# Performance work log

Hardware: AMD Instinct MI355X
Metric: run time of the kernel (lower is better)

The kernel has to match this reference:

```python
import jax, jax.numpy as jnp
import numpy as np

B, C, H, W = 4, 256, 64, 64

def _conv1x1(x, w, b):
    # x: [B,C,H,W], w: [O,C] (1x1 conv kernel squeezed), b: [O]
    return jnp.einsum('bchw,oc->bohw', x, w) + b[None, :, None, None]

def setup_inputs() -> dict:
    key = jax.random.key(0)
    ks = jax.random.split(key, 9)
    s = 1.0 / np.sqrt(C)
    inp = {'x': jax.random.normal(ks[0], (B, C, H, W), dtype=jnp.float32)}
    for i, name in enumerate(['f', 'g', 'h', 'v']):
        inp['W' + name] = jax.random.uniform(ks[1 + 2 * i], (C, C), jnp.float32, -s, s)
        inp['b' + name] = jax.random.uniform(ks[2 + 2 * i], (C,), jnp.float32, -s, s)
    return inp

def reference(x, Wf, bf, Wg, bg, Wh, bh, Wv, bv):
    b, c, h, w = x.shape
    n = h * w
    f = _conv1x1(x, Wf, bf).reshape(b, c, n)  # [B,C,N]
    g = _conv1x1(x, Wg, bg).reshape(b, c, n)  # [B,C,N]
    hh = _conv1x1(x, Wh, bh).reshape(b, c, n)  # [B,C,N]
    fg = jnp.einsum('bci,bcj->bij', f, g)      # [B,N,N], no scaling (as in source)
    attn = jax.nn.softmax(fg, axis=1)          # softmax over dim=1 (first N axis)
    fgh = jnp.einsum('bci,bij->bcj', hh, attn) # [B,C,N]
    return _conv1x1(fgh.reshape(b, c, h, w), Wv, bv)
```

## Files before the change

kernel.cpp:

```cpp
#include <hip/hip_runtime.h>
#include <hip/hip_bf16.h>


typedef short short8 __attribute__((ext_vector_type(8)));
typedef short short4v __attribute__((ext_vector_type(4)));
typedef float f32x4 __attribute__((ext_vector_type(4)));
typedef _Float16 f16x8 __attribute__((ext_vector_type(8)));
typedef unsigned short u16;
typedef unsigned int u32;

#define DEV static __device__ __forceinline__
#define MFMA16(a, b, c) __builtin_amdgcn_mfma_f32_16x16x32_f16(a, b, c, 0, 0, 0)

DEV u16 h16(float x) {
    union { _Float16 h; u16 u; } c;
    c.h = (_Float16)x;
    return c.u;
}
DEV f16x8 ldh8(const u16* p) { return *reinterpret_cast<const f16x8*>(p); }

DEV u32 cvtpk(float a, float b) {
    u32 r;
    asm("v_cvt_pkrtz_f16_f32 %0, %1, %2" : "=v"(r) : "v"(a), "v"(b));
    return r;
}

DEV void gload16(const void* g, void* l) {
    __builtin_amdgcn_global_load_lds(
        (const __attribute__((address_space(1))) unsigned int*)g,
        (__attribute__((address_space(3))) unsigned int*)l, 16, 0, 0);
}

constexpr size_t OFF_WF = 0;
constexpr size_t OFF_WG = 131072;
constexpr size_t OFF_WH = 262144;
constexpr size_t OFF_WV = 393216;
constexpr size_t OFF_ML = 524288;
constexpr size_t OFF_F  = 1310720;
constexpr size_t OFF_G  = OFF_F + 8388608;
constexpr size_t OFF_H  = OFF_G + 8388608;
constexpr size_t OFF_XT = OFF_H + 8388608;
constexpr size_t OFF_OP = OFF_XT;
constexpr size_t OFF_OT = OFF_F;

__global__ __launch_bounds__(256) void k_prep_w(
    const float* __restrict__ Wf, const float* __restrict__ Wg,
    const float* __restrict__ Wh, const float* __restrict__ Wv,
    u16* WF, u16* WG, u16* WH, u16* WV) {
    int i = blockIdx.x * 256 + threadIdx.x;
    WF[i] = h16(Wf[i]);
    WG[i] = h16(Wg[i]);
    WH[i] = h16(Wh[i]);
    WV[i] = h16(Wv[i]);
}

__global__ __launch_bounds__(256) void k_prep_x(const float* __restrict__ x, u16* Xt) {
    __shared__ float lds[64][65];
    int bid = blockIdx.x;
    int b = bid >> 8, rem = bid & 255, ct = rem >> 6, nt = rem & 63;
    int tid = threadIdx.x;
    int tx = tid & 63, ty = tid >> 6;
    const float* src = x + ((size_t)(b * 256 + ct * 64)) * 4096 + nt * 64;
#pragma unroll
    for (int k = 0; k < 16; ++k) {
        int cl = ty * 16 + k;
        lds[cl][tx] = src[(size_t)cl * 4096 + tx];
    }
    __syncthreads();
    int nl = tid >> 2, cg = tid & 3;
    short8 h0, h1;
#pragma unroll
    for (int j = 0; j < 8; ++j) h0[j] = (short)h16(lds[cg * 16 + j][nl]);
#pragma unroll
    for (int j = 8; j < 16; ++j) h1[j - 8] = (short)h16(lds[cg * 16 + j][nl]);
    size_t dst = ((size_t)(b * 4096 + nt * 64 + nl)) * 256 + ct * 64 + cg * 16;
    *reinterpret_cast<short8*>(Xt + dst) = h0;
    *reinterpret_cast<short8*>(Xt + dst + 8) = h1;
}

__global__ __launch_bounds__(256) void k_conv_fg(
    const u16* __restrict__ Xt, const u16* __restrict__ WF, const u16* __restrict__ WG,
    const float* __restrict__ bf, const float* __restrict__ bg,
    u16* F, u16* G) {
    int bidm = blockIdx.x & 255, bido = blockIdx.x >> 8;
    int w = threadIdx.x >> 6, lane = threadIdx.x & 63, r = lane & 15, g = lane >> 4;
    int m0 = bidm * 64 + w * 16, o0 = bido * 64;
    f32x4 fa[4], ga[4];
#pragma unroll
    for (int i = 0; i < 4; ++i) { fa[i] = {0.f, 0.f, 0.f, 0.f}; ga[i] = {0.f, 0.f, 0.f, 0.f}; }
    const u16* ar = Xt + (size_t)(m0 + r) * 256;
#pragma unroll
    for (int ks = 0; ks < 8; ++ks) {
        int k0 = ks * 32 + 8 * g;
        f16x8 a = ldh8(ar + k0);
#pragma unroll
        for (int ot = 0; ot < 4; ++ot) {
            size_t wrow = (size_t)(o0 + ot * 16 + r) * 256 + k0;
            fa[ot] = MFMA16(a, ldh8(WF + wrow), fa[ot]);
            ga[ot] = MFMA16(a, ldh8(WG + wrow), ga[ot]);
        }
    }
#pragma unroll
    for (int ot = 0; ot < 4; ++ot) {
#pragma unroll
        for (int q = 0; q < 4; ++q) {
            int row = m0 + 4 * g + q;
            int col = o0 + ot * 16 + r;
            size_t idx = (size_t)row * 256 + col;
            F[idx] = h16(fa[ot][q] + bf[col]);
            G[idx] = h16(ga[ot][q] + bg[col]);
        }
    }
}

__global__ __launch_bounds__(256) void k_conv_h(
    const u16* __restrict__ WH, const u16* __restrict__ Xt,
    const float* __restrict__ bh, u16* Hb) {
    int bidn = blockIdx.x & 255, bido = blockIdx.x >> 8;
    int w = threadIdx.x >> 6, lane = threadIdx.x & 63, r = lane & 15, g = lane >> 4;
    int o0 = bido * 64 + w * 16, n0 = bidn * 64;
    f32x4 acc[4];
#pragma unroll
    for (int i = 0; i < 4; ++i) acc[i] = {0.f, 0.f, 0.f, 0.f};
    const u16* arow = WH + (size_t)(o0 + r) * 256;
#pragma unroll
    for (int ks = 0; ks < 8; ++ks) {
        int k0 = ks * 32 + 8 * g;
        f16x8 a = ldh8(arow + k0);
#pragma unroll
        for (int ntl = 0; ntl < 4; ++ntl) {
            f16x8 bb = ldh8(Xt + (size_t)(n0 + ntl * 16 + r) * 256 + k0);
            acc[ntl] = MFMA16(a, bb, acc[ntl]);
        }
    }
#pragma unroll
    for (int ntl = 0; ntl < 4; ++ntl) {
#pragma unroll
        for (int q = 0; q < 4; ++q) {
            int o = o0 + 4 * g + q;
            int nf = n0 + ntl * 16 + r;
            int bb = nf >> 12, n = nf & 4095;
            int k5 = n & 31;
            int kp = (k5 < 16) ? (8 * (k5 >> 2) + (k5 & 3))
                               : (8 * ((k5 - 16) >> 2) + 4 + (k5 & 3));
            int np = (n & ~31) | kp;
            Hb[((size_t)(bb * 256 + o)) * 4096 + np] = h16(acc[ntl][q] + bh[o]);
        }
    }
}

__global__ __launch_bounds__(256, 2) void k_attn(
    const u16* __restrict__ F, const u16* __restrict__ G,
    const u16* __restrict__ Hb, u16* __restrict__ OP, float* __restrict__ ML) {
    __shared__ u16 Kd[2][8192];
    __shared__ u16 Vd[2][8192];

    int bid = blockIdx.x;
    int xcd = bid & 7, idx = bid >> 3;
    int b = xcd >> 1, ks = xcd & 1;
    int tid = threadIdx.x;
    int w = tid >> 6, lane = tid & 63, r = lane & 15, g = lane >> 4;
    int j0 = idx * 64 + w * 16;
    const float L2E = 1.4426950408889634f;

    int vlc = (r >> 1) * 128 + (((16 * g) + (r & 1) * 64) ^ (((r >> 1) & 7) << 4));

    f16x8 Qf[8];
    {
        const u16* q = G + (size_t)(b * 4096 + j0 + r) * 256;
#pragma unroll
        for (int k = 0; k < 8; ++k) Qf[k] = ldh8(q + k * 32 + 8 * g);
    }
    f32x4 O[16];
#pragma unroll
    for (int i = 0; i < 16; ++i) O[i] = {0.f, 0.f, 0.f, 0.f};
    float m = -1e30f, l = 0.f;

    const char* Fb  = (const char*)(F + (size_t)b * 4096 * 256);
    const char* Hbb = (const char*)(Hb + (size_t)b * 256 * 4096);

    int ksrc[4], vsrc[4];
#pragma unroll
    for (int t = 0; t < 4; ++t) {
        int d = (w * 4 + t) * 1024 + lane * 16;
        int row = d >> 9, col = d & 511;
        ksrc[t] = row * 512 + (col ^ ((row & 7) << 4));
        int r128 = d >> 7, wn = d & 127;
        int wp = wn ^ ((r128 & 7) << 4);
        vsrc[t] = ((r128 * 2 + (wp >> 6)) << 13) + (wp & 63);
    }

#define STAGE(bufn, I0)                                                         \
    do {                                                                        \
        const char* kb_ = Fb + (size_t)(I0) * 512;                              \
        const char* vb_ = Hbb + (size_t)(I0) * 2;                               \
        char* kl = (char*)Kd[bufn];                                             \
        char* vl = (char*)Vd[bufn];                                             \
        _Pragma("unroll") for (int t = 0; t < 4; ++t)                           \
            gload16(kb_ + ksrc[t], kl + (w * 4 + t) * 1024);                    \
        _Pragma("unroll") for (int t = 0; t < 4; ++t)                           \
            gload16(vb_ + vsrc[t], vl + (w * 4 + t) * 1024);                    \
    } while (0)

    int i0beg = ks * 2048;
    STAGE(0, i0beg);
    __syncthreads();

    for (int it = 0; it < 64; ++it) {
        int cur = it & 1;
        if (it + 1 < 64) STAGE(cur ^ 1, i0beg + (it + 1) * 32);

        const char* Kl = (const char*)Kd[cur];
        const char* Vb = (const char*)Vd[cur] + vlc;

        f32x4 s0 = {0.f, 0.f, 0.f, 0.f};
        f32x4 s1 = {0.f, 0.f, 0.f, 0.f};
        __builtin_amdgcn_s_setprio(1);
        {
            const char* kr = Kl + r * 512;
            int sw = (r & 7) << 4;
#pragma unroll
            for (int k = 0; k < 8; ++k) {
                f16x8 ka = *reinterpret_cast<const f16x8*>(kr + ((k * 64 + 16 * g) ^ sw));
                s0 = MFMA16(ka, Qf[k], s0);
            }
        }
        {
            const char* kr = Kl + (16 + r) * 512;
            int sw = (r & 7) << 4;
#pragma unroll
            for (int k = 0; k < 8; ++k) {
                f16x8 ka = *reinterpret_cast<const f16x8*>(kr + ((k * 64 + 16 * g) ^ sw));
                s1 = MFMA16(ka, Qf[k], s1);
            }
        }
        __builtin_amdgcn_s_setprio(0);

        float v = fmaxf(fmaxf(fmaxf(s0[0], s0[1]), fmaxf(s0[2], s0[3])),
                        fmaxf(fmaxf(s1[0], s1[1]), fmaxf(s1[2], s1[3])));
        v = fmaxf(v, __shfl_xor(v, 16));
        v = fmaxf(v, __shfl_xor(v, 32));
        float grow = v - m;
        if (__all(grow <= 8.0f)) {
#pragma unroll
            for (int q = 0; q < 4; ++q) {
                s0[q] = exp2f((s0[q] - m) * L2E);
                s1[q] = exp2f((s1[q] - m) * L2E);
            }
            l += (s0[0] + s0[1] + s0[2] + s0[3]) + (s1[0] + s1[1] + s1[2] + s1[3]);
        } else {
            float mn = fmaxf(m, v);
            float corr = exp2f((m - mn) * L2E);
            m = mn;
#pragma unroll
            for (int q = 0; q < 4; ++q) {
                s0[q] = exp2f((s0[q] - m) * L2E);
                s1[q] = exp2f((s1[q] - m) * L2E);
            }
            l = l * corr + (s0[0] + s0[1] + s0[2] + s0[3]) + (s1[0] + s1[1] + s1[2] + s1[3]);
#pragma unroll
            for (int ct = 0; ct < 16; ++ct) O[ct] *= corr;
        }

        union { u32 wd[4]; f16x8 fr; } pu;
        pu.wd[0] = cvtpk(s0[0], s0[1]);
        pu.wd[1] = cvtpk(s0[2], s0[3]);
        pu.wd[2] = cvtpk(s1[0], s1[1]);
        pu.wd[3] = cvtpk(s1[2], s1[3]);

        __builtin_amdgcn_s_setprio(1);
#pragma unroll
        for (int ct = 0; ct < 16; ++ct) {
            f16x8 vb = *reinterpret_cast<const f16x8*>(Vb + ct * 1024);
            O[ct] = MFMA16(vb, pu.fr, O[ct]);
        }
        __builtin_amdgcn_s_setprio(0);

        __syncthreads();
    }
#undef STAGE

    l += __shfl_xor(l, 16);
    l += __shfl_xor(l, 32);
    float inv = 1.f / l;
    size_t mrow = (size_t)ks * 16384 + b * 4096 + j0 + r;
#pragma unroll
    for (int ct = 0; ct < 16; ++ct) {
        short4v pk;
#pragma unroll
        for (int q = 0; q < 4; ++q) pk[q] = (short)h16(O[ct][q] * inv);
        *reinterpret_cast<short4v*>(OP + mrow * 256 + ct * 16 + 4 * g) = pk;
    }
    if (g == 0) {
        size_t mi = mrow * 2;
        ML[mi] = m;
        ML[mi + 1] = l;
    }
}

__global__ __launch_bounds__(256) void k_merge(
    const u16* __restrict__ OP, const float* __restrict__ ML, u16* __restrict__ OT) {
    int t = blockIdx.x * 256 + threadIdx.x;
    int m = t >> 5;
    int c0 = (t & 31) * 8;
    const float L2E = 1.4426950408889634f;
    float m0 = ML[(size_t)m * 2], l0 = ML[(size_t)m * 2 + 1];
    float m1 = ML[((size_t)16384 + m) * 2], l1 = ML[((size_t)16384 + m) * 2 + 1];
    float M = fmaxf(m0, m1);
    float wl0 = exp2f((m0 - M) * L2E) * l0;
    float wl1 = exp2f((m1 - M) * L2E) * l1;
    float inv = 1.f / (wl0 + wl1);
    f16x8 v0 = ldh8(OP + (size_t)m * 256 + c0);
    f16x8 v1 = ldh8(OP + ((size_t)16384 + m) * 256 + c0);
    short8 outp;
#pragma unroll
    for (int j = 0; j < 8; ++j)
        outp[j] = (short)h16((wl0 * (float)v0[j] + wl1 * (float)v1[j]) * inv);
    *reinterpret_cast<short8*>(OT + (size_t)m * 256 + c0) = outp;
}

__global__ __launch_bounds__(256) void k_conv_out(
    const u16* __restrict__ WV, const u16* __restrict__ OT,
    const float* __restrict__ bv, float* __restrict__ out) {
    int bidn = blockIdx.x & 255, bido = blockIdx.x >> 8;
    int w = threadIdx.x >> 6, lane = threadIdx.x & 63, r = lane & 15, g = lane >> 4;
    int o0 = bido * 64 + w * 16, n0 = bidn * 64;
    f32x4 acc[4];
#pragma unroll
    for (int i = 0; i < 4; ++i) acc[i] = {0.f, 0.f, 0.f, 0.f};
    const u16* arow = WV + (size_t)(o0 + r) * 256;
#pragma unroll
    for (int ks = 0; ks < 8; ++ks) {
        int k0 = ks * 32 + 8 * g;
        f16x8 a = ldh8(arow + k0);
#pragma unroll
        for (int ntl = 0; ntl < 4; ++ntl) {
            f16x8 bb = ldh8(OT + (size_t)(n0 + ntl * 16 + r) * 256 + k0);
            acc[ntl] = MFMA16(a, bb, acc[ntl]);
        }
    }
#pragma unroll
    for (int ntl = 0; ntl < 4; ++ntl) {
#pragma unroll
        for (int q = 0; q < 4; ++q) {
            int o = o0 + 4 * g + q;
            int nf = n0 + ntl * 16 + r;
            int bb = nf >> 12, n = nf & 4095;
            out[((size_t)(bb * 256 + o)) * 4096 + n] = acc[ntl][q] + bv[o];
        }
    }
}

extern "C" void kernel_launch(void* const* d_in, const int* in_sizes, int n_in,
                              void* d_out, int out_size, void* d_ws, size_t ws_size,
                              hipStream_t stream) {
    const float* x  = (const float*)d_in[0];
    const float* Wf = (const float*)d_in[1];
    const float* bf = (const float*)d_in[2];
    const float* Wg = (const float*)d_in[3];
    const float* bg = (const float*)d_in[4];
    const float* Wh = (const float*)d_in[5];
    const float* bh = (const float*)d_in[6];
    const float* Wv = (const float*)d_in[7];
    const float* bv = (const float*)d_in[8];
    float* out = (float*)d_out;
    char* ws = (char*)d_ws;

    u16* WF = (u16*)(ws + OFF_WF);
    u16* WG = (u16*)(ws + OFF_WG);
    u16* WH = (u16*)(ws + OFF_WH);
    u16* WV = (u16*)(ws + OFF_WV);
    float* ML = (float*)(ws + OFF_ML);
    u16* F  = (u16*)(ws + OFF_F);
    u16* G  = (u16*)(ws + OFF_G);
    u16* H  = (u16*)(ws + OFF_H);
    u16* XT = (u16*)(ws + OFF_XT);
    u16* OP = (u16*)(ws + OFF_OP);
    u16* OT = (u16*)(ws + OFF_OT);

    k_prep_w<<<256, 256, 0, stream>>>(Wf, Wg, Wh, Wv, WF, WG, WH, WV);
    k_prep_x<<<1024, 256, 0, stream>>>(x, XT);
    k_conv_fg<<<1024, 256, 0, stream>>>(XT, WF, WG, bf, bg, F, G);
    k_conv_h<<<1024, 256, 0, stream>>>(WH, XT, bh, H);
    k_attn<<<512, 256, 0, stream>>>(F, G, H, OP, ML);
    k_merge<<<2048, 256, 0, stream>>>(OP, ML, OT);
    k_conv_out<<<1024, 256, 0, stream>>>(WV, OT, bv, out);
}
```

Before: 214.0 us.

## Fold Wf and Wg into one matrix and fuse the split merge into the output conv

```diff
diff --git a/kernel.cpp b/kernel.cpp
--- a/kernel.cpp
+++ b/kernel.cpp
@@ -31,27 +31,39 @@
         (__attribute__((address_space(3))) unsigned int*)l, 16, 0, 0);
 }
 
-constexpr size_t OFF_WF = 0;
-constexpr size_t OFF_WG = 131072;
-constexpr size_t OFF_WH = 262144;
-constexpr size_t OFF_WV = 393216;
-constexpr size_t OFF_ML = 524288;
-constexpr size_t OFF_F  = 1310720;
-constexpr size_t OFF_G  = OFF_F + 8388608;
-constexpr size_t OFF_H  = OFF_G + 8388608;
+constexpr size_t OFF_WH = 0;
+constexpr size_t OFF_WV = 131072;
+constexpr size_t OFF_MB = 262144;
+constexpr size_t OFF_ML = 266240;
+constexpr size_t OFF_M  = 524288;
+constexpr size_t OFF_U  = 1310720;
+constexpr size_t OFF_H  = OFF_U + 8388608;
 constexpr size_t OFF_XT = OFF_H + 8388608;
-constexpr size_t OFF_OP = OFF_XT;
-constexpr size_t OFF_OT = OFF_F;
+constexpr size_t OFF_OP = OFF_XT + 8388608;
 
 __global__ __launch_bounds__(256) void k_prep_w(
-    const float* __restrict__ Wf, const float* __restrict__ Wg,
-    const float* __restrict__ Wh, const float* __restrict__ Wv,
-    u16* WF, u16* WG, u16* WH, u16* WV) {
+    const float* __restrict__ Wh, const float* __restrict__ Wv, u16* WH, u16* WV) {
     int i = blockIdx.x * 256 + threadIdx.x;
-    WF[i] = h16(Wf[i]);
-    WG[i] = h16(Wg[i]);
     WH[i] = h16(Wh[i]);
     WV[i] = h16(Wv[i]);
+}
+
+__global__ __launch_bounds__(256) void k_gemm_M(
+    const float* __restrict__ Wf, const float* __restrict__ Wg,
+    const float* __restrict__ bg, u16* __restrict__ M, float* __restrict__ Mb) {
+    int c = blockIdx.x;
+    int t = threadIdx.x;
+    __shared__ float wf[256];
+    wf[t] = Wf[(size_t)t * 256 + c];
+    __syncthreads();
+    float acc = 0.f;
+    for (int o = 0; o < 256; ++o) acc += wf[o] * Wg[(size_t)o * 256 + t];
+    M[(size_t)c * 256 + t] = h16(acc);
+    if (t == 0) {
+        float s = 0.f;
+        for (int o = 0; o < 256; ++o) s += wf[o] * bg[o];
+        Mb[c] = s;
+    }
 }
 
 __global__ __launch_bounds__(256) void k_prep_x(const float* __restrict__ x, u16* Xt) {
@@ -78,16 +90,15 @@
     *reinterpret_cast<short8*>(Xt + dst + 8) = h1;
 }
 
-__global__ __launch_bounds__(256) void k_conv_fg(
-    const u16* __restrict__ Xt, const u16* __restrict__ WF, const u16* __restrict__ WG,
-    const float* __restrict__ bf, const float* __restrict__ bg,
-    u16* F, u16* G) {
+__global__ __launch_bounds__(256) void k_conv_u(
+    const u16* __restrict__ Xt, const u16* __restrict__ M,
+    const float* __restrict__ Mb, u16* U) {
     int bidm = blockIdx.x & 255, bido = blockIdx.x >> 8;
     int w = threadIdx.x >> 6, lane = threadIdx.x & 63, r = lane & 15, g = lane >> 4;
     int m0 = bidm * 64 + w * 16, o0 = bido * 64;
-    f32x4 fa[4], ga[4];
-#pragma unroll
-    for (int i = 0; i < 4; ++i) { fa[i] = {0.f, 0.f, 0.f, 0.f}; ga[i] = {0.f, 0.f, 0.f, 0.f}; }
+    f32x4 ua[4];
+#pragma unroll
+    for (int i = 0; i < 4; ++i) ua[i] = {0.f, 0.f, 0.f, 0.f};
     const u16* ar = Xt + (size_t)(m0 + r) * 256;
 #pragma unroll
     for (int ks = 0; ks < 8; ++ks) {
@@ -96,8 +107,7 @@
 #pragma unroll
         for (int ot = 0; ot < 4; ++ot) {
             size_t wrow = (size_t)(o0 + ot * 16 + r) * 256 + k0;
-            fa[ot] = MFMA16(a, ldh8(WF + wrow), fa[ot]);
-            ga[ot] = MFMA16(a, ldh8(WG + wrow), ga[ot]);
+            ua[ot] = MFMA16(a, ldh8(M + wrow), ua[ot]);
         }
     }
 #pragma unroll
@@ -106,9 +116,7 @@
         for (int q = 0; q < 4; ++q) {
             int row = m0 + 4 * g + q;
             int col = o0 + ot * 16 + r;
-            size_t idx = (size_t)row * 256 + col;
-            F[idx] = h16(fa[ot][q] + bf[col]);
-            G[idx] = h16(ga[ot][q] + bg[col]);
+            U[(size_t)row * 256 + col] = h16(ua[ot][q] + Mb[col]);
         }
     }
 }
@@ -298,33 +306,29 @@
     }
 }
 
-__global__ __launch_bounds__(256) void k_merge(
-    const u16* __restrict__ OP, const float* __restrict__ ML, u16* __restrict__ OT) {
-    int t = blockIdx.x * 256 + threadIdx.x;
-    int m = t >> 5;
-    int c0 = (t & 31) * 8;
-    const float L2E = 1.4426950408889634f;
-    float m0 = ML[(size_t)m * 2], l0 = ML[(size_t)m * 2 + 1];
-    float m1 = ML[((size_t)16384 + m) * 2], l1 = ML[((size_t)16384 + m) * 2 + 1];
-    float M = fmaxf(m0, m1);
-    float wl0 = exp2f((m0 - M) * L2E) * l0;
-    float wl1 = exp2f((m1 - M) * L2E) * l1;
-    float inv = 1.f / (wl0 + wl1);
-    f16x8 v0 = ldh8(OP + (size_t)m * 256 + c0);
-    f16x8 v1 = ldh8(OP + ((size_t)16384 + m) * 256 + c0);
-    short8 outp;
-#pragma unroll
-    for (int j = 0; j < 8; ++j)
-        outp[j] = (short)h16((wl0 * (float)v0[j] + wl1 * (float)v1[j]) * inv);
-    *reinterpret_cast<short8*>(OT + (size_t)m * 256 + c0) = outp;
-}
-
 __global__ __launch_bounds__(256) void k_conv_out(
-    const u16* __restrict__ WV, const u16* __restrict__ OT,
-    const float* __restrict__ bv, float* __restrict__ out) {
+    const u16* __restrict__ WV, const u16* __restrict__ OP,
+    const float* __restrict__ ML, const float* __restrict__ bv,
+    float* __restrict__ out) {
     int bidn = blockIdx.x & 255, bido = blockIdx.x >> 8;
     int w = threadIdx.x >> 6, lane = threadIdx.x & 63, r = lane & 15, g = lane >> 4;
     int o0 = bido * 64 + w * 16, n0 = bidn * 64;
+    const float L2E = 1.4426950408889634f;
+    float wl0[4], wl1[4];
+    int nfs[4];
+#pragma unroll
+    for (int ntl = 0; ntl < 4; ++ntl) {
+        int nf = n0 + ntl * 16 + r;
+        nfs[ntl] = nf;
+        float m0_ = ML[(size_t)nf * 2], l0_ = ML[(size_t)nf * 2 + 1];
+        float m1_ = ML[((size_t)16384 + nf) * 2], l1_ = ML[((size_t)16384 + nf) * 2 + 1];
+        float M_ = fmaxf(m0_, m1_);
+        float a0 = exp2f((m0_ - M_) * L2E) * l0_;
+        float a1 = exp2f((m1_ - M_) * L2E) * l1_;
+        float inv = 1.f / (a0 + a1);
+        wl0[ntl] = a0 * inv;
+        wl1[ntl] = a1 * inv;
+    }
     f32x4 acc[4];
 #pragma unroll
     for (int i = 0; i < 4; ++i) acc[i] = {0.f, 0.f, 0.f, 0.f};
@@ -335,8 +339,16 @@
         f16x8 a = ldh8(arow + k0);
 #pragma unroll
         for (int ntl = 0; ntl < 4; ++ntl) {
-            f16x8 bb = ldh8(OT + (size_t)(n0 + ntl * 16 + r) * 256 + k0);
-            acc[ntl] = MFMA16(a, bb, acc[ntl]);
+            f16x8 v0 = ldh8(OP + (size_t)nfs[ntl] * 256 + k0);
+            f16x8 v1 = ldh8(OP + ((size_t)16384 + nfs[ntl]) * 256 + k0);
+            union { u32 wd[4]; f16x8 fr; } bb;
+#pragma unroll
+            for (int j = 0; j < 4; ++j) {
+                float e0 = wl0[ntl] * (float)v0[2 * j] + wl1[ntl] * (float)v1[2 * j];
+                float e1 = wl0[ntl] * (float)v0[2 * j + 1] + wl1[ntl] * (float)v1[2 * j + 1];
+                bb.wd[j] = cvtpk(e0, e1);
+            }
+            acc[ntl] = MFMA16(a, bb.fr, acc[ntl]);
         }
     }
 #pragma unroll
@@ -344,9 +356,9 @@
 #pragma unroll
         for (int q = 0; q < 4; ++q) {
             int o = o0 + 4 * g + q;
-            int nf = n0 + ntl * 16 + r;
-            int bb = nf >> 12, n = nf & 4095;
-            out[((size_t)(bb * 256 + o)) * 4096 + n] = acc[ntl][q] + bv[o];
+            int nf = nfs[ntl] - r + r;
+            int bb2 = nf >> 12, n = nf & 4095;
+            out[((size_t)(bb2 * 256 + o)) * 4096 + n] = acc[ntl][q] + bv[o];
         }
     }
 }
@@ -365,24 +377,23 @@
     const float* bv = (const float*)d_in[8];
     float* out = (float*)d_out;
     char* ws = (char*)d_ws;
-
-    u16* WF = (u16*)(ws + OFF_WF);
-    u16* WG = (u16*)(ws + OFF_WG);
+    (void)bf;
+
     u16* WH = (u16*)(ws + OFF_WH);
     u16* WV = (u16*)(ws + OFF_WV);
+    float* MB = (float*)(ws + OFF_MB);
     float* ML = (float*)(ws + OFF_ML);
-    u16* F  = (u16*)(ws + OFF_F);
-    u16* G  = (u16*)(ws + OFF_G);
+    u16* M  = (u16*)(ws + OFF_M);
+    u16* U  = (u16*)(ws + OFF_U);
     u16* H  = (u16*)(ws + OFF_H);
     u16* XT = (u16*)(ws + OFF_XT);
     u16* OP = (u16*)(ws + OFF_OP);
-    u16* OT = (u16*)(ws + OFF_OT);
-
-    k_prep_w<<<256, 256, 0, stream>>>(Wf, Wg, Wh, Wv, WF, WG, WH, WV);
+
+    k_prep_w<<<256, 256, 0, stream>>>(Wh, Wv, WH, WV);
+    k_gemm_M<<<256, 256, 0, stream>>>(Wf, Wg, bg, M, MB);
     k_prep_x<<<1024, 256, 0, stream>>>(x, XT);
-    k_conv_fg<<<1024, 256, 0, stream>>>(XT, WF, WG, bf, bg, F, G);
+    k_conv_u<<<1024, 256, 0, stream>>>(XT, M, MB, U);
     k_conv_h<<<1024, 256, 0, stream>>>(WH, XT, bh, H);
-    k_attn<<<512, 256, 0, stream>>>(F, G, H, OP, ML);
-    k_merge<<<2048, 256, 0, stream>>>(OP, ML, OT);
-    k_conv_out<<<1024, 256, 0, stream>>>(WV, OT, bv, out);
-}
+    k_attn<<<512, 256, 0, stream>>>(XT, U, H, OP, ML);
+    k_conv_out<<<1024, 256, 0, stream>>>(WV, OP, ML, bv, out);
+}
```

After: 216.6 us. No clear change (+1.3%).
